# Kernel optimization log

Measured on AMD Instinct MI355X. Metric: run time of the kernel, lower is better.

Reference implementation:

```python
import jax, jax.numpy as jnp
import numpy as np

G, S, M = 4, 2048, 1024   # groups (batch), tokens per group, emb dim
E, H, K = 8, 4096, 2      # experts, mlp dim, top-k
CAP = int(K * S / E * 1.25)  # expert capacity = 640
AUX_COEF, Z_COEF = 0.01, 0.001


def setup_inputs() -> dict:
    key = jax.random.key(0)
    k1, k2, k3, k4, k5 = jax.random.split(key, 5)
    return {
        "inputs": jax.random.normal(k1, (G, S, M), jnp.float32),
        "paddings": jnp.zeros((G, S), jnp.float32),  # 1.0 = padded token
        "router_w": jax.random.normal(k2, (M, E), jnp.float32) / np.sqrt(M),
        "wi_gate": jax.random.normal(k3, (E, M, H), jnp.float32) / np.sqrt(M),
        "wi_0": jax.random.normal(k4, (E, M, H), jnp.float32) / np.sqrt(M),
        "wo": jax.random.normal(k5, (E, H, M), jnp.float32) / np.sqrt(H),
    }


def reference(inputs, paddings, router_w, wi_gate, wi_0, wo):
    # Router
    logits = jnp.einsum('gsm,me->gse', inputs, router_w)          # [G,S,E]
    probs = jax.nn.softmax(logits, axis=-1)
    top_p, top_i = jax.lax.top_k(probs, K)                        # [G,S,K]

    nonpad = 1.0 - paddings                                       # [G,S]
    exp_mask = jax.nn.one_hot(top_i, E, dtype=jnp.float32)        # [G,S,K,E]
    exp_mask = exp_mask * nonpad[:, :, None, None]

    # Position in expert (capacity-limited), priority by token order then k slot
    mask_flat = exp_mask.reshape(G, S * K, E)
    pos = jnp.cumsum(mask_flat, axis=1) * mask_flat               # 1-indexed where assigned
    keep = mask_flat * (pos <= CAP)
    pos_oh = jax.nn.one_hot((pos - 1.0).astype(jnp.int32), CAP, dtype=jnp.float32)  # [G,SK,E,CAP]
    dispatch_k = (keep[..., None] * pos_oh).reshape(G, S, K, E, CAP)
    dispatch = dispatch_k.sum(axis=2)                             # [G,S,E,CAP]
    combine = jnp.einsum('gsk,gskec->gsec', top_p, dispatch_k)    # [G,S,E,CAP]

    # Dispatch -> gated expert FFN -> combine
    expert_in = jnp.einsum('gsec,gsm->egcm', dispatch, inputs)    # [E,G,CAP,M]
    h = jax.nn.silu(jnp.einsum('egcm,emh->egch', expert_in, wi_gate)) \
        * jnp.einsum('egcm,emh->egch', expert_in, wi_0)           # [E,G,CAP,H]
    expert_out = jnp.einsum('egch,ehm->egcm', h, wo)              # [E,G,CAP,M]
    output = jnp.einsum('gsec,egcm->gsm', combine, expert_out)    # [G,S,M]

    # Aux losses: load-balancing (Switch style) + router z-loss
    em = jnp.max(jax.nn.one_hot(top_i, E, dtype=jnp.float32), axis=-2)       # [G,S,E]
    lb = jnp.mean(jnp.mean(em, axis=-2) * jnp.mean(probs, axis=-2)) * E * E
    z = jnp.mean(jax.nn.logsumexp(logits, axis=-1) ** 2)
    aux_loss = AUX_COEF * lb + Z_COEF * z
    return output, aux_loss
```

## Files before the change

### kernel.cpp

```cpp
#include <hip/hip_runtime.h>
#include <hip/hip_bf16.h>
#include <math.h>

#define G 4
#define S 2048
#define MDIM 1024
#define E 8
#define HDIM 4096
#define TOPK 2
#define CAP 640
#define GC (G*CAP)

typedef __attribute__((ext_vector_type(8))) short bf16x8;
typedef __attribute__((ext_vector_type(4))) short s16x4;
typedef __attribute__((ext_vector_type(4))) float f32x4;
typedef unsigned int u32;
typedef unsigned short u16;

#define MFMA16(a,b,c) __builtin_amdgcn_mfma_f32_16x16x32_bf16(a,b,c,0,0,0)

__device__ __forceinline__ u16 f2bf(float f) {
    union { float f; u32 u; } v; v.f = f;
    u32 r = v.u + 0x7fffu + ((v.u >> 16) & 1u);
    return (u16)(r >> 16);
}

__device__ __forceinline__ void gload16(const char* gp, char* lp) {
    __builtin_amdgcn_global_load_lds((const __attribute__((address_space(1))) u32*)gp,
                                     (__attribute__((address_space(3))) u32*)lp,
                                     16, 0, 0);
}

__device__ __forceinline__ int swzb(int r) { return ((r >> 1) & 3) << 4; }

__global__ __launch_bounds__(256) void transpose_cvt(const float* __restrict__ in,
                                                     u16* __restrict__ out, int R, int C) {
    int e = blockIdx.z;
    const float* ine = in + (size_t)e * R * C;
    u16* oute = out + (size_t)e * R * C;
    __shared__ float tile[32][33];
    int tx = threadIdx.x, ty = threadIdx.y;
    int x0 = blockIdx.x * 32, y0 = blockIdx.y * 32;
    #pragma unroll
    for (int i = 0; i < 4; ++i)
        tile[ty + i*8][tx] = ine[(size_t)(y0 + ty + i*8) * C + x0 + tx];
    __syncthreads();
    #pragma unroll
    for (int i = 0; i < 4; ++i)
        oute[(size_t)(x0 + ty + i*8) * R + y0 + tx] = f2bf(tile[tx][ty + i*8]);
}

__global__ __launch_bounds__(256) void router_kernel(const float* __restrict__ inp,
                                                     const float* __restrict__ rw,
                                                     int* __restrict__ top_i,
                                                     float* __restrict__ top_p,
                                                     float* __restrict__ partials) {
    int wid = threadIdx.x >> 6, lane = threadIdx.x & 63;
    int tok = blockIdx.x * 4 + wid;
    const float* x = inp + (size_t)tok * MDIM;
    float acc[E] = {0.f,0.f,0.f,0.f,0.f,0.f,0.f,0.f};
    #pragma unroll
    for (int rep = 0; rep < 4; ++rep) {
        int m0 = rep * 256 + lane * 4;
        f32x4 xv = *(const f32x4*)(x + m0);
        #pragma unroll
        for (int j = 0; j < 4; ++j) {
            const float* r = rw + (size_t)(m0 + j) * E;
            float xj = xv[j];
            #pragma unroll
            for (int e = 0; e < E; ++e) acc[e] += xj * r[e];
        }
    }
    #pragma unroll
    for (int e = 0; e < E; ++e)
        #pragma unroll
        for (int off = 32; off; off >>= 1) acc[e] += __shfl_down(acc[e], off);

    __shared__ float part[4][17];
    if (lane == 0) {
        float mx = acc[0];
        #pragma unroll
        for (int e = 1; e < E; ++e) mx = fmaxf(mx, acc[e]);
        float p[E], sum = 0.f;
        #pragma unroll
        for (int e = 0; e < E; ++e) { p[e] = expf(acc[e] - mx); sum += p[e]; }
        float inv = 1.f / sum;
        #pragma unroll
        for (int e = 0; e < E; ++e) p[e] *= inv;
        float lse = logf(sum) + mx;
        int i0 = 0;
        #pragma unroll
        for (int e = 1; e < E; ++e) if (acc[e] > acc[i0]) i0 = e;
        int i1 = (i0 == 0) ? 1 : 0;
        #pragma unroll
        for (int e = 0; e < E; ++e) if (e != i0 && acc[e] > acc[i1]) i1 = e;
        top_i[tok*2+0] = i0; top_i[tok*2+1] = i1;
        top_p[tok*2+0] = p[i0]; top_p[tok*2+1] = p[i1];
        #pragma unroll
        for (int e = 0; e < E; ++e) { part[wid][e] = p[e]; part[wid][8+e] = 0.f; }
        part[wid][8+i0] = 1.f; part[wid][8+i1] = 1.f;
        part[wid][16] = lse * lse;
    }
    __syncthreads();
    if (threadIdx.x < 17) {
        float v = part[0][threadIdx.x] + part[1][threadIdx.x] +
                  part[2][threadIdx.x] + part[3][threadIdx.x];
        partials[(size_t)blockIdx.x * 17 + threadIdx.x] = v;
    }
}

__global__ __launch_bounds__(256) void reduce_partials(const float* __restrict__ partials,
                                                       float* __restrict__ sums) {
    int g = blockIdx.x, t = threadIdx.x;
    float loc[17];
    #pragma unroll
    for (int c = 0; c < 17; ++c) loc[c] = 0.f;
    for (int r = t; r < 1024; r += 256) {
        const float* pr = partials + ((size_t)g * 1024 + r) * 17;
        #pragma unroll
        for (int c = 0; c < 17; ++c) loc[c] += pr[c];
    }
    __shared__ float red[256];
    for (int c = 0; c < 17; ++c) {
        red[t] = loc[c]; __syncthreads();
        for (int off = 128; off; off >>= 1) {
            if (t < off) red[t] += red[t + off];
            __syncthreads();
        }
        if (t == 0) sums[g * 17 + c] = red[0];
        __syncthreads();
    }
}

__global__ void aux_final(const float* __restrict__ sums, float* __restrict__ out) {
    float lb = 0.f, z = 0.f;
    for (int g = 0; g < G; ++g) {
        for (int e = 0; e < E; ++e)
            lb += (sums[g*17 + 8 + e] / (float)S) * (sums[g*17 + e] / (float)S);
        z += sums[g*17 + 16];
    }
    lb = lb / (float)(G * E) * (float)(E * E);
    z /= (float)(G * S);
    out[(size_t)G * S * MDIM] = 0.01f * lb + 0.001f * z;
}

__global__ __launch_bounds__(256) void scan_kernel(const int* __restrict__ top_i,
                                                   const float* __restrict__ pad,
                                                   int* __restrict__ slot_token,
                                                   int* __restrict__ token_c) {
    int b = blockIdx.x; int g = b >> 3, e = b & 7;
    int t = threadIdx.x;
    __shared__ int sums[256];
    int base = t * 16;
    int run = 0; unsigned mask16 = 0; int loc[16];
    #pragma unroll
    for (int j = 0; j < 16; ++j) {
        int i = base + j; int s = i >> 1, k = i & 1;
        int ex = top_i[((size_t)(g * S + s)) * 2 + k];
        int m = (ex == e) && (pad[g * S + s] == 0.f);
        run += m; loc[j] = run; mask16 |= ((unsigned)m << j);
    }
    sums[t] = run; __syncthreads();
    for (int off = 1; off < 256; off <<= 1) {
        int v = (t >= off) ? sums[t - off] : 0;
        __syncthreads();
        sums[t] += v;
        __syncthreads();
    }
    int excl = sums[t] - run;
    #pragma unroll
    for (int j = 0; j < 16; ++j) {
        if ((mask16 >> j) & 1u) {
            int pos = excl + loc[j];
            if (pos <= CAP) {
                int i = base + j; int s = i >> 1, k = i & 1;
                slot_token[((size_t)(e * G + g)) * CAP + (pos - 1)] = s;
                token_c[((size_t)(g * S + s)) * 2 + k] = pos - 1;
            }
        }
    }
}

__global__ __launch_bounds__(128) void gather_kernel(const float* __restrict__ inp,
                                                     const int* __restrict__ slot_token,
                                                     u16* __restrict__ X) {
    int row = blockIdx.x;
    int t = threadIdx.x;
    int s = slot_token[row];
    int g = (row % GC) / CAP;
    bf16x8 v;
    if (s >= 0) {
        const float* src = inp + ((size_t)(g * S + s)) * MDIM + t * 8;
        f32x4 a = *(const f32x4*)src;
        f32x4 b = *(const f32x4*)(src + 4);
        #pragma unroll
        for (int j = 0; j < 4; ++j) { v[j] = (short)f2bf(a[j]); v[4+j] = (short)f2bf(b[j]); }
    } else {
        #pragma unroll
        for (int j = 0; j < 8; ++j) v[j] = 0;
    }
    *(bf16x8*)(X + (size_t)row * MDIM + t * 8) = v;
}

__global__ __launch_bounds__(512, 2) void gemm_ffn12_v2(
        const u16* __restrict__ Xb, const u16* __restrict__ WgT,
        const u16* __restrict__ W0T, u16* __restrict__ Hb) {
    extern __shared__ char smem[];
    const int NK = MDIM / 32;
    int bid = blockIdx.x;
    int swz = (bid & 7) * 320 + (bid >> 3);
    int mt = swz % 10, nt = (swz / 10) & 31, e = swz / 320;
    const char* A  = (const char*)(Xb  + (size_t)e * GC * MDIM   + (size_t)mt * 256 * MDIM);
    const char* Bg = (const char*)(WgT + (size_t)e * HDIM * MDIM + (size_t)nt * 128 * MDIM);
    const char* B0 = (const char*)(W0T + (size_t)e * HDIM * MDIM + (size_t)nt * 128 * MDIM);
    int tid = threadIdx.x, w = tid >> 6, l = tid & 63;
    int wm = w >> 2, wn = w & 3;
    int rl = l >> 2, cch = (l & 3) * 16;
    int fr = l & 15, fg = l >> 4;

    f32x4 ag[8][2], ao[8][2];
    #pragma unroll
    for (int i = 0; i < 8; ++i) {
        ag[i][0] = (f32x4){0,0,0,0}; ag[i][1] = (f32x4){0,0,0,0};
        ao[i][0] = (f32x4){0,0,0,0}; ao[i][1] = (f32x4){0,0,0,0};
    }

    auto stageA = [&](int t) {
        char* dst = smem + (t & 3) * 16384;
        #pragma unroll
        for (int i = 0; i < 2; ++i) {
            int r = (i * 8 + w) * 16 + rl;
            gload16(A + ((size_t)r * MDIM + t * 32) * 2 + (cch ^ swzb(r)),
                    dst + (i * 8 + w) * 1024);
        }
    };
    auto stageB = [&](int t) {
        int r = w * 16 + rl;
        gload16(Bg + ((size_t)r * MDIM + t * 32) * 2 + (cch ^ swzb(r)),
                smem + 65536 + (t & 3) * 8192 + w * 1024);
        gload16(B0 + ((size_t)r * MDIM + t * 32) * 2 + (cch ^ swzb(r)),
                smem + 98304 + (t & 3) * 8192 + w * 1024);
    };
    auto ldA = [&](int fm, int t) -> bf16x8 {
        int r = wm * 128 + fm * 16 + fr;
        return *(const bf16x8*)(smem + (t & 3) * 16384 + r * 64 + ((fg * 16) ^ swzb(r)));
    };
    auto ldG = [&](int fn, int t) -> bf16x8 {
        int r = wn * 32 + fn * 16 + fr;
        return *(const bf16x8*)(smem + 65536 + (t & 3) * 8192 + r * 64 + ((fg * 16) ^ swzb(r)));
    };
    auto ldO = [&](int fn, int t) -> bf16x8 {
        int r = wn * 32 + fn * 16 + fr;
        return *(const bf16x8*)(smem + 98304 + (t & 3) * 8192 + r * 64 + ((fg * 16) ^ swzb(r)));
    };

    stageA(0); stageB(0);
    stageA(1); stageB(1);
    asm volatile("s_waitcnt vmcnt(4)" ::: "memory");
    __builtin_amdgcn_s_barrier();

    #pragma unroll 1
    for (int t = 0; t < NK; ++t) {
        bf16x8 af[4], bgf[2], bof[2];
        #pragma unroll
        for (int i = 0; i < 4; ++i) af[i] = ldA(i, t);
        bgf[0] = ldG(0, t); bgf[1] = ldG(1, t);
        bof[0] = ldO(0, t); bof[1] = ldO(1, t);
        if (t + 2 < NK) stageA(t + 2);
        __builtin_amdgcn_s_barrier();
        asm volatile("s_waitcnt lgkmcnt(0)" ::: "memory");
        __builtin_amdgcn_sched_barrier(0);
        __builtin_amdgcn_s_setprio(1);
        #pragma unroll
        for (int fm = 0; fm < 4; ++fm)
            #pragma unroll
            for (int fn = 0; fn < 2; ++fn) {
                ag[fm][fn] = MFMA16(bgf[fn], af[fm], ag[fm][fn]);
                ao[fm][fn] = MFMA16(bof[fn], af[fm], ao[fm][fn]);
            }
        __builtin_amdgcn_s_setprio(0);
        __builtin_amdgcn_s_barrier();
        bf16x8 af2[4];
        #pragma unroll
        for (int i = 0; i < 4; ++i) af2[i] = ldA(4 + i, t);
        if (t + 2 < NK) {
            stageB(t + 2);
            asm volatile("s_waitcnt vmcnt(4)" ::: "memory");
        } else {
            asm volatile("s_waitcnt vmcnt(0)" ::: "memory");
        }
        __builtin_amdgcn_s_barrier();
        asm volatile("s_waitcnt lgkmcnt(0)" ::: "memory");
        __builtin_amdgcn_sched_barrier(0);
        __builtin_amdgcn_s_setprio(1);
        #pragma unroll
        for (int fm = 0; fm < 4; ++fm)
            #pragma unroll
            for (int fn = 0; fn < 2; ++fn) {
                ag[4+fm][fn] = MFMA16(bgf[fn], af2[fm], ag[4+fm][fn]);
                ao[4+fm][fn] = MFMA16(bof[fn], af2[fm], ao[4+fm][fn]);
            }
        __builtin_amdgcn_s_setprio(0);
        __builtin_amdgcn_s_barrier();
    }

    u16* He = Hb + (size_t)e * GC * HDIM;
    int row0 = mt * 256 + wm * 128 + fr;
    int col0 = nt * 128 + wn * 32 + fg * 4;
    #pragma unroll
    for (int fm = 0; fm < 8; ++fm)
        #pragma unroll
        for (int fn = 0; fn < 2; ++fn) {
            s16x4 pk;
            #pragma unroll
            for (int r = 0; r < 4; ++r) {
                float gv = ag[fm][fn][r], ov = ao[fm][fn][r];
                float hv = gv / (1.f + __expf(-gv)) * ov;
                pk[r] = (short)f2bf(hv);
            }
            *(s16x4*)(He + (size_t)(row0 + fm * 16) * HDIM + col0 + fn * 16) = pk;
        }
}

__global__ __launch_bounds__(512, 2) void gemm_out_v2(
        const u16* __restrict__ Hb, const u16* __restrict__ WoT,
        float* __restrict__ EO) {
    extern __shared__ char smem[];
    const int NK = HDIM / 32;
    int bid = blockIdx.x;
    int swz = (bid & 7) * 80 + (bid >> 3);
    int nt = swz & 3, mt = (swz / 4) % 20, e = swz / 80;
    const char* A = (const char*)(Hb  + (size_t)e * GC * HDIM   + (size_t)mt * 128 * HDIM);
    const char* B = (const char*)(WoT + (size_t)e * MDIM * HDIM + (size_t)nt * 256 * HDIM);
    int tid = threadIdx.x, w = tid >> 6, l = tid & 63;
    int wm = w >> 2, wn = w & 3;
    int rl = l >> 2, cch = (l & 3) * 16;
    int fr = l & 15, fg = l >> 4;

    f32x4 acc[4][4];
    #pragma unroll
    for (int i = 0; i < 4; ++i)
        #pragma unroll
        for (int j = 0; j < 4; ++j) acc[i][j] = (f32x4){0,0,0,0};

    auto stageA = [&](int t) {
        int r = w * 16 + rl;
        gload16(A + ((size_t)r * HDIM + t * 32) * 2 + (cch ^ swzb(r)),
                smem + (t & 3) * 8192 + w * 1024);
    };
    auto stageB = [&](int t) {
        char* dst = smem + 32768 + (t & 3) * 16384;
        #pragma unroll
        for (int i = 0; i < 2; ++i) {
            int r = (i * 8 + w) * 16 + rl;
            gload16(B + ((size_t)r * HDIM + t * 32) * 2 + (cch ^ swzb(r)),
                    dst + (i * 8 + w) * 1024);
        }
    };
    auto ldA = [&](int fm, int t) -> bf16x8 {
        int r = wm * 64 + fm * 16 + fr;
        return *(const bf16x8*)(smem + (t & 3) * 8192 + r * 64 + ((fg * 16) ^ swzb(r)));
    };
    auto ldB = [&](int fn, int t) -> bf16x8 {
        int r = wn * 64 + fn * 16 + fr;
        return *(const bf16x8*)(smem + 32768 + (t & 3) * 16384 + r * 64 + ((fg * 16) ^ swzb(r)));
    };

    stageA(0); stageB(0);
    stageA(1); stageB(1);
    asm volatile("s_waitcnt vmcnt(3)" ::: "memory");
    __builtin_amdgcn_s_barrier();

    #pragma unroll 1
    for (int t = 0; t < NK; ++t) {
        bf16x8 af[4], bf[4];
        #pragma unroll
        for (int i = 0; i < 4; ++i) { af[i] = ldA(i, t); bf[i] = ldB(i, t); }
        if (t + 2 < NK) {
            stageA(t + 2); stageB(t + 2);
            asm volatile("s_waitcnt vmcnt(3)" ::: "memory");
        } else {
            asm volatile("s_waitcnt vmcnt(0)" ::: "memory");
        }
        __builtin_amdgcn_s_barrier();
        asm volatile("s_waitcnt lgkmcnt(0)" ::: "memory");
        __builtin_amdgcn_sched_barrier(0);
        __builtin_amdgcn_s_setprio(1);
        #pragma unroll
        for (int fm = 0; fm < 4; ++fm)
            #pragma unroll
            for (int fn = 0; fn < 4; ++fn)
                acc[fm][fn] = MFMA16(bf[fn], af[fm], acc[fm][fn]);
        __builtin_amdgcn_s_setprio(0);
        __builtin_amdgcn_s_barrier();
    }

    float* Ee = EO + (size_t)e * GC * MDIM;
    int row0 = mt * 128 + wm * 64 + fr;
    int col0 = nt * 256 + wn * 64 + fg * 4;
    #pragma unroll
    for (int fm = 0; fm < 4; ++fm)
        #pragma unroll
        for (int fn = 0; fn < 4; ++fn)
            *(f32x4*)(Ee + (size_t)(row0 + fm * 16) * MDIM + col0 + fn * 16) = acc[fm][fn];
}

__global__ __launch_bounds__(256) void combine_kernel(const float* __restrict__ EO,
                                                      const int* __restrict__ top_i,
                                                      const float* __restrict__ top_p,
                                                      const int* __restrict__ token_c,
                                                      float* __restrict__ out) {
    int tok = blockIdx.x, t = threadIdx.x;
    int g = tok >> 11;
    f32x4 acc = {0.f, 0.f, 0.f, 0.f};
    #pragma unroll
    for (int k = 0; k < 2; ++k) {
        int c = token_c[tok * 2 + k];
        if (c >= 0) {
            int e = top_i[tok * 2 + k];
            float p = top_p[tok * 2 + k];
            const float* src = EO + ((size_t)e * GC + g * CAP + c) * MDIM + t * 4;
            f32x4 v = *(const f32x4*)src;
            #pragma unroll
            for (int j = 0; j < 4; ++j) acc[j] += p * v[j];
        }
    }
    *(f32x4*)(out + (size_t)tok * MDIM + t * 4) = acc;
}

extern "C" void kernel_launch(void* const* d_in, const int* in_sizes, int n_in,
                              void* d_out, int out_size, void* d_ws, size_t ws_size,
                              hipStream_t stream) {
    (void)in_sizes; (void)n_in; (void)out_size; (void)ws_size;
    const float* inputs   = (const float*)d_in[0];
    const float* paddings = (const float*)d_in[1];
    const float* router_w = (const float*)d_in[2];
    const float* wi_gate  = (const float*)d_in[3];
    const float* wi_0     = (const float*)d_in[4];
    const float* wo       = (const float*)d_in[5];
    float* out = (float*)d_out;

    char* p = (char*)d_ws;
    u16* WgT = (u16*)p; p += (size_t)E * HDIM * MDIM * 2;
    u16* W0T = (u16*)p; p += (size_t)E * HDIM * MDIM * 2;
    u16* WoT = (u16*)p; p += (size_t)E * HDIM * MDIM * 2;
    u16* Xb  = (u16*)p; p += (size_t)E * GC * MDIM * 2;
    u16* Hb  = (u16*)p; p += (size_t)E * GC * HDIM * 2;
    float* EO = (float*)p; p += (size_t)E * GC * MDIM * 4;
    int*   top_i = (int*)p;   p += (size_t)G * S * TOPK * 4;
    float* top_p = (float*)p; p += (size_t)G * S * TOPK * 4;
    int*   token_c = (int*)p; p += (size_t)G * S * TOPK * 4;
    int*   slot_token = (int*)p; p += (size_t)E * G * CAP * 4;
    float* partials = (float*)p; p += (size_t)4096 * 17 * 4;
    float* sums = (float*)p; p += 4 * 17 * 4;

    hipMemsetAsync(token_c, 0xFF, (size_t)G * S * TOPK * 4, stream);
    hipMemsetAsync(slot_token, 0xFF, (size_t)E * G * CAP * 4, stream);

    hipFuncSetAttribute((const void*)gemm_ffn12_v2,
                        hipFuncAttributeMaxDynamicSharedMemorySize, 131072);
    hipFuncSetAttribute((const void*)gemm_out_v2,
                        hipFuncAttributeMaxDynamicSharedMemorySize, 98304);

    transpose_cvt<<<dim3(HDIM/32, MDIM/32, E), dim3(32, 8), 0, stream>>>(wi_gate, WgT, MDIM, HDIM);
    transpose_cvt<<<dim3(HDIM/32, MDIM/32, E), dim3(32, 8), 0, stream>>>(wi_0,   W0T, MDIM, HDIM);
    transpose_cvt<<<dim3(MDIM/32, HDIM/32, E), dim3(32, 8), 0, stream>>>(wo,     WoT, HDIM, MDIM);

    router_kernel<<<G * S / 4, 256, 0, stream>>>(inputs, router_w, top_i, top_p, partials);
    reduce_partials<<<G, 256, 0, stream>>>(partials, sums);
    scan_kernel<<<G * E, 256, 0, stream>>>(top_i, paddings, slot_token, token_c);
    gather_kernel<<<E * GC, 128, 0, stream>>>(inputs, slot_token, Xb);
    gemm_ffn12_v2<<<2560, 512, 131072, stream>>>(Xb, WgT, W0T, Hb);
    gemm_out_v2<<<640, 512, 98304, stream>>>(Hb, WoT, EO);
    combine_kernel<<<G * S, 256, 0, stream>>>(EO, top_i, top_p, token_c, out);
    aux_final<<<1, 1, 0, stream>>>(sums, out);
}
```

Before: 832.9 us.

## Restructure expert GEMM main loops with precomputed addresses and register double-buffering

```diff
diff --git a/kernel.cpp b/kernel.cpp
--- a/kernel.cpp
+++ b/kernel.cpp
@@ -202,7 +202,7 @@
     *(bf16x8*)(X + (size_t)row * MDIM + t * 8) = v;
 }
 
-__global__ __launch_bounds__(512, 2) void gemm_ffn12_v2(
+__global__ __launch_bounds__(512, 1) void gemm_ffn12_v4(
         const u16* __restrict__ Xb, const u16* __restrict__ WgT,
         const u16* __restrict__ W0T, u16* __restrict__ Hb) {
     extern __shared__ char smem[];
@@ -217,6 +217,15 @@
     int wm = w >> 2, wn = w & 3;
     int rl = l >> 2, cch = (l & 3) * 16;
     int fr = l & 15, fg = l >> 4;
+    int lswz = ((fr >> 1) & 3) << 4;
+
+    int rA0 = (0 * 8 + w) * 16 + rl, rA1 = (1 * 8 + w) * 16 + rl, rB = w * 16 + rl;
+    const char* gA0 = A  + (size_t)rA0 * MDIM * 2 + (cch ^ swzb(rA0));
+    const char* gA1 = A  + (size_t)rA1 * MDIM * 2 + (cch ^ swzb(rA1));
+    const char* gBg = Bg + (size_t)rB  * MDIM * 2 + (cch ^ swzb(rB));
+    const char* gB0 = B0 + (size_t)rB  * MDIM * 2 + (cch ^ swzb(rB));
+    int baseA = (wm * 128 + fr) * 64 + ((fg * 16) ^ lswz);
+    int baseB = (wn * 32  + fr) * 64 + ((fg * 16) ^ lswz);
 
     f32x4 ag[8][2], ao[8][2];
     #pragma unroll
@@ -225,83 +234,43 @@
         ao[i][0] = (f32x4){0,0,0,0}; ao[i][1] = (f32x4){0,0,0,0};
     }
 
-    auto stageA = [&](int t) {
-        char* dst = smem + (t & 3) * 16384;
-        #pragma unroll
-        for (int i = 0; i < 2; ++i) {
-            int r = (i * 8 + w) * 16 + rl;
-            gload16(A + ((size_t)r * MDIM + t * 32) * 2 + (cch ^ swzb(r)),
-                    dst + (i * 8 + w) * 1024);
-        }
+    auto stage = [&](int tt) {
+        int kk = tt * 64, b = tt & 3;
+        gload16(gA0 + kk, smem + b * 16384 + (0 * 8 + w) * 1024);
+        gload16(gA1 + kk, smem + b * 16384 + (1 * 8 + w) * 1024);
+        gload16(gBg + kk, smem + 65536 + b * 8192 + w * 1024);
+        gload16(gB0 + kk, smem + 98304 + b * 8192 + w * 1024);
     };
-    auto stageB = [&](int t) {
-        int r = w * 16 + rl;
-        gload16(Bg + ((size_t)r * MDIM + t * 32) * 2 + (cch ^ swzb(r)),
-                smem + 65536 + (t & 3) * 8192 + w * 1024);
-        gload16(B0 + ((size_t)r * MDIM + t * 32) * 2 + (cch ^ swzb(r)),
-                smem + 98304 + (t & 3) * 8192 + w * 1024);
-    };
-    auto ldA = [&](int fm, int t) -> bf16x8 {
-        int r = wm * 128 + fm * 16 + fr;
-        return *(const bf16x8*)(smem + (t & 3) * 16384 + r * 64 + ((fg * 16) ^ swzb(r)));
-    };
-    auto ldG = [&](int fn, int t) -> bf16x8 {
-        int r = wn * 32 + fn * 16 + fr;
-        return *(const bf16x8*)(smem + 65536 + (t & 3) * 8192 + r * 64 + ((fg * 16) ^ swzb(r)));
-    };
-    auto ldO = [&](int fn, int t) -> bf16x8 {
-        int r = wn * 32 + fn * 16 + fr;
-        return *(const bf16x8*)(smem + 98304 + (t & 3) * 8192 + r * 64 + ((fg * 16) ^ swzb(r)));
-    };
-
-    stageA(0); stageB(0);
-    stageA(1); stageB(1);
-    asm volatile("s_waitcnt vmcnt(4)" ::: "memory");
-    __builtin_amdgcn_s_barrier();
+
+    stage(0); stage(1);
 
     #pragma unroll 1
     for (int t = 0; t < NK; ++t) {
-        bf16x8 af[4], bgf[2], bof[2];
-        #pragma unroll
-        for (int i = 0; i < 4; ++i) af[i] = ldA(i, t);
-        bgf[0] = ldG(0, t); bgf[1] = ldG(1, t);
-        bof[0] = ldO(0, t); bof[1] = ldO(1, t);
-        if (t + 2 < NK) stageA(t + 2);
+        if (t + 2 < NK) {
+            stage(t + 2);
+            asm volatile("s_waitcnt vmcnt(4)" ::: "memory");
+        } else {
+            asm volatile("s_waitcnt vmcnt(0)" ::: "memory");
+        }
         __builtin_amdgcn_s_barrier();
-        asm volatile("s_waitcnt lgkmcnt(0)" ::: "memory");
         __builtin_amdgcn_sched_barrier(0);
+        const char* bufA = smem + (t & 3) * 16384;
+        const char* pG = smem + 65536 + (t & 3) * 8192 + baseB;
+        const char* pO = smem + 98304 + (t & 3) * 8192 + baseB;
+        bf16x8 bgf[2], bof[2], af[8];
+        bgf[0] = *(const bf16x8*)(pG);  bgf[1] = *(const bf16x8*)(pG + 1024);
+        bof[0] = *(const bf16x8*)(pO);  bof[1] = *(const bf16x8*)(pO + 1024);
+        #pragma unroll
+        for (int fm = 0; fm < 8; ++fm) af[fm] = *(const bf16x8*)(bufA + baseA + fm * 1024);
         __builtin_amdgcn_s_setprio(1);
         #pragma unroll
-        for (int fm = 0; fm < 4; ++fm)
+        for (int fm = 0; fm < 8; ++fm)
             #pragma unroll
             for (int fn = 0; fn < 2; ++fn) {
                 ag[fm][fn] = MFMA16(bgf[fn], af[fm], ag[fm][fn]);
                 ao[fm][fn] = MFMA16(bof[fn], af[fm], ao[fm][fn]);
             }
         __builtin_amdgcn_s_setprio(0);
-        __builtin_amdgcn_s_barrier();
-        bf16x8 af2[4];
-        #pragma unroll
-        for (int i = 0; i < 4; ++i) af2[i] = ldA(4 + i, t);
-        if (t + 2 < NK) {
-            stageB(t + 2);
-            asm volatile("s_waitcnt vmcnt(4)" ::: "memory");
-        } else {
-            asm volatile("s_waitcnt vmcnt(0)" ::: "memory");
-        }
-        __builtin_amdgcn_s_barrier();
-        asm volatile("s_waitcnt lgkmcnt(0)" ::: "memory");
-        __builtin_amdgcn_sched_barrier(0);
-        __builtin_amdgcn_s_setprio(1);
-        #pragma unroll
-        for (int fm = 0; fm < 4; ++fm)
-            #pragma unroll
-            for (int fn = 0; fn < 2; ++fn) {
-                ag[4+fm][fn] = MFMA16(bgf[fn], af2[fm], ag[4+fm][fn]);
-                ao[4+fm][fn] = MFMA16(bof[fn], af2[fm], ao[4+fm][fn]);
-            }
-        __builtin_amdgcn_s_setprio(0);
-        __builtin_amdgcn_s_barrier();
     }
 
     u16* He = Hb + (size_t)e * GC * HDIM;
@@ -322,7 +291,7 @@
         }
 }
 
-__global__ __launch_bounds__(512, 2) void gemm_out_v2(
+__global__ __launch_bounds__(512, 1) void gemm_out_v4(
         const u16* __restrict__ Hb, const u16* __restrict__ WoT,
         float* __restrict__ EO) {
     extern __shared__ char smem[];
@@ -336,6 +305,14 @@
     int wm = w >> 2, wn = w & 3;
     int rl = l >> 2, cch = (l & 3) * 16;
     int fr = l & 15, fg = l >> 4;
+    int lswz = ((fr >> 1) & 3) << 4;
+
+    int rA = w * 16 + rl, rB0 = (0 * 8 + w) * 16 + rl, rB1 = (1 * 8 + w) * 16 + rl;
+    const char* gA  = A + (size_t)rA  * HDIM * 2 + (cch ^ swzb(rA));
+    const char* gBa = B + (size_t)rB0 * HDIM * 2 + (cch ^ swzb(rB0));
+    const char* gBb = B + (size_t)rB1 * HDIM * 2 + (cch ^ swzb(rB1));
+    int baseA = (wm * 64 + fr) * 64 + ((fg * 16) ^ lswz);
+    int baseB = (wn * 64 + fr) * 64 + ((fg * 16) ^ lswz);
 
     f32x4 acc[4][4];
     #pragma unroll
@@ -343,56 +320,61 @@
         #pragma unroll
         for (int j = 0; j < 4; ++j) acc[i][j] = (f32x4){0,0,0,0};
 
-    auto stageA = [&](int t) {
-        int r = w * 16 + rl;
-        gload16(A + ((size_t)r * HDIM + t * 32) * 2 + (cch ^ swzb(r)),
-                smem + (t & 3) * 8192 + w * 1024);
+    auto stage = [&](int tt) {
+        int kk = tt * 64, b = tt & 3;
+        gload16(gA  + kk, smem + b * 8192 + w * 1024);
+        gload16(gBa + kk, smem + 32768 + b * 16384 + (0 * 8 + w) * 1024);
+        gload16(gBb + kk, smem + 32768 + b * 16384 + (1 * 8 + w) * 1024);
     };
-    auto stageB = [&](int t) {
-        char* dst = smem + 32768 + (t & 3) * 16384;
-        #pragma unroll
-        for (int i = 0; i < 2; ++i) {
-            int r = (i * 8 + w) * 16 + rl;
-            gload16(B + ((size_t)r * HDIM + t * 32) * 2 + (cch ^ swzb(r)),
-                    dst + (i * 8 + w) * 1024);
-        }
-    };
-    auto ldA = [&](int fm, int t) -> bf16x8 {
-        int r = wm * 64 + fm * 16 + fr;
-        return *(const bf16x8*)(smem + (t & 3) * 8192 + r * 64 + ((fg * 16) ^ swzb(r)));
-    };
-    auto ldB = [&](int fn, int t) -> bf16x8 {
-        int r = wn * 64 + fn * 16 + fr;
-        return *(const bf16x8*)(smem + 32768 + (t & 3) * 16384 + r * 64 + ((fg * 16) ^ swzb(r)));
-    };
-
-    stageA(0); stageB(0);
-    stageA(1); stageB(1);
+
+    bf16x8 afA[4], bfA[4], afB[4], bfB[4];
+
+    stage(0); stage(1);
     asm volatile("s_waitcnt vmcnt(3)" ::: "memory");
     __builtin_amdgcn_s_barrier();
-
-    #pragma unroll 1
-    for (int t = 0; t < NK; ++t) {
-        bf16x8 af[4], bf[4];
-        #pragma unroll
-        for (int i = 0; i < 4; ++i) { af[i] = ldA(i, t); bf[i] = ldB(i, t); }
+    __builtin_amdgcn_sched_barrier(0);
+    {
+        const char* pA = smem + baseA;
+        const char* pB = smem + 32768 + baseB;
+        #pragma unroll
+        for (int i = 0; i < 4; ++i) {
+            afA[i] = *(const bf16x8*)(pA + i * 1024);
+            bfA[i] = *(const bf16x8*)(pB + i * 1024);
+        }
+    }
+
+    auto body = [&](int t, bf16x8 (&afc)[4], bf16x8 (&bfc)[4],
+                    bf16x8 (&afn)[4], bf16x8 (&bfn)[4]) {
         if (t + 2 < NK) {
-            stageA(t + 2); stageB(t + 2);
+            stage(t + 2);
             asm volatile("s_waitcnt vmcnt(3)" ::: "memory");
         } else {
             asm volatile("s_waitcnt vmcnt(0)" ::: "memory");
         }
         __builtin_amdgcn_s_barrier();
-        asm volatile("s_waitcnt lgkmcnt(0)" ::: "memory");
         __builtin_amdgcn_sched_barrier(0);
+        if (t + 1 < NK) {
+            const char* pA = smem + ((t + 1) & 3) * 8192 + baseA;
+            const char* pB = smem + 32768 + ((t + 1) & 3) * 16384 + baseB;
+            #pragma unroll
+            for (int i = 0; i < 4; ++i) {
+                afn[i] = *(const bf16x8*)(pA + i * 1024);
+                bfn[i] = *(const bf16x8*)(pB + i * 1024);
+            }
+        }
         __builtin_amdgcn_s_setprio(1);
         #pragma unroll
         for (int fm = 0; fm < 4; ++fm)
             #pragma unroll
             for (int fn = 0; fn < 4; ++fn)
-                acc[fm][fn] = MFMA16(bf[fn], af[fm], acc[fm][fn]);
+                acc[fm][fn] = MFMA16(bfc[fn], afc[fm], acc[fm][fn]);
         __builtin_amdgcn_s_setprio(0);
-        __builtin_amdgcn_s_barrier();
+    };
+
+    #pragma unroll 1
+    for (int t = 0; t < NK; t += 2) {
+        body(t, afA, bfA, afB, bfB);
+        body(t + 1, afB, bfB, afA, bfA);
     }
 
     float* Ee = EO + (size_t)e * GC * MDIM;
@@ -457,9 +439,9 @@
     hipMemsetAsync(token_c, 0xFF, (size_t)G * S * TOPK * 4, stream);
     hipMemsetAsync(slot_token, 0xFF, (size_t)E * G * CAP * 4, stream);
 
-    hipFuncSetAttribute((const void*)gemm_ffn12_v2,
+    hipFuncSetAttribute((const void*)gemm_ffn12_v4,
                         hipFuncAttributeMaxDynamicSharedMemorySize, 131072);
-    hipFuncSetAttribute((const void*)gemm_out_v2,
+    hipFuncSetAttribute((const void*)gemm_out_v4,
                         hipFuncAttributeMaxDynamicSharedMemorySize, 98304);
 
     transpose_cvt<<<dim3(HDIM/32, MDIM/32, E), dim3(32, 8), 0, stream>>>(wi_gate, WgT, MDIM, HDIM);
@@ -470,8 +452,8 @@
     reduce_partials<<<G, 256, 0, stream>>>(partials, sums);
     scan_kernel<<<G * E, 256, 0, stream>>>(top_i, paddings, slot_token, token_c);
     gather_kernel<<<E * GC, 128, 0, stream>>>(inputs, slot_token, Xb);
-    gemm_ffn12_v2<<<2560, 512, 131072, stream>>>(Xb, WgT, W0T, Hb);
-    gemm_out_v2<<<640, 512, 98304, stream>>>(Hb, WoT, EO);
+    gemm_ffn12_v4<<<2560, 512, 131072, stream>>>(Xb, WgT, W0T, Hb);
+    gemm_out_v4<<<640, 512, 98304, stream>>>(Hb, WoT, EO);
     combine_kernel<<<G * S, 256, 0, stream>>>(EO, top_i, top_p, token_c, out);
     aux_final<<<1, 1, 0, stream>>>(sums, out);
 }
```

New measurement: 802.5 us. -3.7%, faster.
